# Optimization experiments

Hardware: AMD Instinct MI355X
Metric: run time of the kernel (lower is better)

Reference implementation:

```python
import jax, jax.numpy as jnp
import numpy as np

N_NODES = 50000
N_EDGES = 600000
IN_DIM = 128
HID_DIM = 512
OUT_DIM = 2


def setup_inputs() -> dict:
    key = jax.random.key(0)
    ks = jax.random.split(key, 8)
    x = jax.random.normal(ks[0], (N_NODES, IN_DIM), dtype=jnp.float32)
    edge_index = jax.random.randint(ks[1], (2, N_EDGES), 0, N_NODES, dtype=jnp.int32)
    s1 = 1.0 / np.sqrt(IN_DIM)
    s2 = 1.0 / np.sqrt(HID_DIM)
    # SAGEConv params: lin_l (applied to mean-aggregated neighbors, has bias),
    # lin_r (applied to root node features, no bias)
    W1l = jax.random.uniform(ks[2], (IN_DIM, HID_DIM), jnp.float32, -s1, s1)
    b1 = jax.random.uniform(ks[3], (HID_DIM,), jnp.float32, -s1, s1)
    W1r = jax.random.uniform(ks[4], (IN_DIM, HID_DIM), jnp.float32, -s1, s1)
    W2l = jax.random.uniform(ks[5], (HID_DIM, OUT_DIM), jnp.float32, -s2, s2)
    b2 = jax.random.uniform(ks[6], (OUT_DIM,), jnp.float32, -s2, s2)
    W2r = jax.random.uniform(ks[7], (HID_DIM, OUT_DIM), jnp.float32, -s2, s2)
    return {"x": x, "W1l": W1l, "b1": b1, "W1r": W1r,
            "W2l": W2l, "b2": b2, "W2r": W2r, "edge_index": edge_index}


def _sage_conv(x, edge_index, Wl, b, Wr):
    src, dst = edge_index[0], edge_index[1]
    msgs = x[src]                                             # [E, d]
    agg = jax.ops.segment_sum(msgs, dst, num_segments=x.shape[0])  # [N, d]
    deg = jax.ops.segment_sum(jnp.ones_like(dst, dtype=x.dtype), dst,
                              num_segments=x.shape[0])
    agg = agg / jnp.maximum(deg, 1.0)[:, None]                # mean aggregation
    return agg @ Wl + b + x @ Wr


def reference(x, W1l, b1, W1r, W2l, b2, W2r, edge_index):
    h = _sage_conv(x, edge_index, W1l, b1, W1r)
    h = jax.nn.relu(h)
    # dropout inactive (eval mode / force_dropout=False)
    out = _sage_conv(h, edge_index, W2l, b2, W2r)
    return jax.nn.log_softmax(out, axis=1)
```

## Files before the change

kernel.cpp:

```cpp
#include <hip/hip_runtime.h>
#include <math.h>
#include <stdint.h>

#define N_NODES 50000
#define N_EDGES 600000
#define IN_DIM 128
#define HID_DIM 512
#define M_PAD 50048
#define SCAN_NB 196

#define CASTX_NB 6250
#define CASTW_NB 544

#define NB_H 64
#define CE4_H 2344
#define NPAD 50048
#define H2_WORDS 25024

typedef __bf16 bf16;
typedef __bf16 bf16x2 __attribute__((ext_vector_type(2)));
typedef __bf16 bf16x4 __attribute__((ext_vector_type(4)));
typedef __bf16 bf16x8 __attribute__((ext_vector_type(8)));
typedef float f32x4 __attribute__((ext_vector_type(4)));

#define GLDS(gp, lp) __builtin_amdgcn_global_load_lds( \
    (const __attribute__((address_space(1))) uint32_t*)(gp), \
    (__attribute__((address_space(3))) uint32_t*)(lp), 16, 0, 0)


__global__ __launch_bounds__(256) void prep_kernel(
    const float* __restrict__ x, bf16* __restrict__ xb,
    const float* __restrict__ W1l, const float* __restrict__ W1r,
    const float* __restrict__ W2l, const float* __restrict__ W2r,
    bf16* __restrict__ Wt, bf16* __restrict__ W2bt) {
    int b = blockIdx.x;
    int t = threadIdx.x;
    if (b < CASTX_NB) {
        int i = b * 256 + t;
        float4 v = ((const float4*)x)[i];
        bf16x4 o = {(bf16)v.x, (bf16)v.y, (bf16)v.z, (bf16)v.w};
        *(bf16x4*)(xb + (size_t)i * 4) = o;
    } else {
        int idx = (b - CASTX_NB) * 256 + t;
        if (idx < 512 * 256) {
            int n = idx >> 8;
            int k = idx & 255;
            float v = (k < IN_DIM) ? W1l[(size_t)k * HID_DIM + n]
                                   : W1r[(size_t)(k - IN_DIM) * HID_DIM + n];
            Wt[idx] = (bf16)v;
        } else {
            int j = idx - 512 * 256;
            int n = j >> 9;
            int k = j & 511;
            float v = 0.f;
            if (n == 0) v = W2l[k * 2 + 0];
            else if (n == 1) v = W2l[k * 2 + 1];
            else if (n == 2) v = W2r[k * 2 + 0];
            else if (n == 3) v = W2r[k * 2 + 1];
            W2bt[j] = (bf16)v;
        }
    }
}


__global__ __launch_bounds__(512) void hist_kernel(
    const int* __restrict__ dst, uint32_t* __restrict__ Hg32) {
    __shared__ uint32_t h2[H2_WORDS];
    int b = blockIdx.x, t = threadIdx.x;
    for (int j = t; j < H2_WORDS; j += 512) h2[j] = 0;
    __syncthreads();
    int e40 = b * CE4_H;
    int e4end = min(e40 + CE4_H, N_EDGES / 4);
    for (int e4 = e40 + t; e4 < e4end; e4 += 512) {
        int4 d = ((const int4*)dst)[e4];
        atomicAdd(&h2[d.x >> 1], 1u << ((d.x & 1) << 4));
        atomicAdd(&h2[d.y >> 1], 1u << ((d.y & 1) << 4));
        atomicAdd(&h2[d.z >> 1], 1u << ((d.z & 1) << 4));
        atomicAdd(&h2[d.w >> 1], 1u << ((d.w & 1) << 4));
    }
    __syncthreads();
    for (int j = t; j < H2_WORDS; j += 512)
        Hg32[(size_t)b * H2_WORDS + j] = h2[j];
}


__global__ __launch_bounds__(256) void scancols_kernel(
    const uint16_t* __restrict__ Hg, int* __restrict__ deg,
    uint16_t* __restrict__ PB, int* __restrict__ bsum) {
    int t = threadIdx.x;
    int n = blockIdx.x * 256 + t;
    int running = 0;
    if (n < NPAD) {
#pragma unroll 4
        for (int b = 0; b < NB_H; ++b) {
            int v = Hg[(size_t)b * NPAD + n];
            PB[(size_t)b * NPAD + n] = (uint16_t)running;
            running += v;
        }
        deg[n] = running;
    }
    int v = (n < N_NODES) ? running : 0;
#pragma unroll
    for (int m = 1; m < 64; m <<= 1) v += __shfl_xor(v, m);
    __shared__ int ws_[4];
    int w = t >> 6, l = t & 63;
    if (l == 0) ws_[w] = v;
    __syncthreads();
    if (t == 0) bsum[blockIdx.x] = ws_[0] + ws_[1] + ws_[2] + ws_[3];
}

__global__ __launch_bounds__(256) void scan3_kernel(const int* __restrict__ deg,
                                                    const int* __restrict__ bsum,
                                                    int* __restrict__ offsets) {
    int t = threadIdx.x;
    int blk = blockIdx.x;
    int i = blk * 256 + t;
    int l = t & 63, w = t >> 6;
    int v = (i < N_NODES) ? deg[i] : 0;
    int inc = v;
#pragma unroll
    for (int off = 1; off < 64; off <<= 1) {
        int y = __shfl_up(inc, off);
        if (l >= off) inc += y;
    }
    __shared__ int wsum[4];
    __shared__ int lookback;
    if (l == 63) wsum[w] = inc;
    __syncthreads();
    if (t < 64) {
        int s = 0;
        for (int u = t; u < blk; u += 64) s += bsum[u];
#pragma unroll
        for (int m = 1; m < 64; m <<= 1) s += __shfl_xor(s, m);
        if (t == 0) lookback = s;
    }
    __syncthreads();
    int add = lookback;
    for (int u = 0; u < w; ++u) add += wsum[u];
    int ex = add + inc - v;
    if (i < N_NODES) offsets[i] = ex;
    if (blk == 0 && t == 0) offsets[N_NODES] = N_EDGES;
}


__global__ __launch_bounds__(512) void fill_kernel(
    const int* __restrict__ src, const int* __restrict__ dst,
    const int* __restrict__ offsets, const uint16_t* __restrict__ PB,
    int* __restrict__ csr_src) {
    __shared__ uint32_t h2[H2_WORDS];
    int b = blockIdx.x, t = threadIdx.x;
    for (int j = t; j < H2_WORDS; j += 512) h2[j] = 0;
    __syncthreads();
    const uint16_t* pb = PB + (size_t)b * NPAD;
    int e40 = b * CE4_H;
    int e4end = min(e40 + CE4_H, N_EDGES / 4);
    for (int e4 = e40 + t; e4 < e4end; e4 += 512) {
        int4 d = ((const int4*)dst)[e4];
        int4 s = ((const int4*)src)[e4];
        int sh0 = (d.x & 1) << 4, sh1 = (d.y & 1) << 4;
        int sh2 = (d.z & 1) << 4, sh3 = (d.w & 1) << 4;
        uint32_t r0 = atomicAdd(&h2[d.x >> 1], 1u << sh0);
        uint32_t r1 = atomicAdd(&h2[d.y >> 1], 1u << sh1);
        uint32_t r2 = atomicAdd(&h2[d.z >> 1], 1u << sh2);
        uint32_t r3 = atomicAdd(&h2[d.w >> 1], 1u << sh3);
        int k0 = (int)((r0 >> sh0) & 0xffff);
        int k1 = (int)((r1 >> sh1) & 0xffff);
        int k2 = (int)((r2 >> sh2) & 0xffff);
        int k3 = (int)((r3 >> sh3) & 0xffff);
        csr_src[offsets[d.x] + (int)pb[d.x] + k0] = s.x;
        csr_src[offsets[d.y] + (int)pb[d.y] + k1] = s.y;
        csr_src[offsets[d.z] + (int)pb[d.z] + k2] = s.z;
        csr_src[offsets[d.w] + (int)pb[d.w] + k3] = s.w;
    }
}


__global__ __launch_bounds__(256) void agg1_kernel(
    const bf16* __restrict__ xb, const int* __restrict__ offsets,
    const int* __restrict__ csr_src, bf16* __restrict__ agg1b) {
    int t = threadIdx.x;
    int w = t >> 6, l = t & 63;
    int g = l >> 4;
    int sl = l & 15;
    int n = blockIdx.x * 16 + w * 4 + g;
    int s0 = offsets[n], s1 = offsets[n + 1];
    float a[8] = {};
    int e = s0;
    for (; e + 4 <= s1; e += 4) {
        int i0 = csr_src[e + 0];
        int i1 = csr_src[e + 1];
        int i2 = csr_src[e + 2];
        int i3 = csr_src[e + 3];
        bf16x8 v0 = *(const bf16x8*)(xb + (size_t)i0 * IN_DIM + sl * 8);
        bf16x8 v1 = *(const bf16x8*)(xb + (size_t)i1 * IN_DIM + sl * 8);
        bf16x8 v2 = *(const bf16x8*)(xb + (size_t)i2 * IN_DIM + sl * 8);
        bf16x8 v3 = *(const bf16x8*)(xb + (size_t)i3 * IN_DIM + sl * 8);
#pragma unroll
        for (int u = 0; u < 8; ++u)
            a[u] += (float)v0[u] + (float)v1[u] + (float)v2[u] + (float)v3[u];
    }
    for (; e < s1; ++e) {
        int i0 = csr_src[e];
        bf16x8 v0 = *(const bf16x8*)(xb + (size_t)i0 * IN_DIM + sl * 8);
#pragma unroll
        for (int u = 0; u < 8; ++u) a[u] += (float)v0[u];
    }
    float inv = 1.0f / fmaxf((float)(s1 - s0), 1.0f);
    bf16x8 o;
#pragma unroll
    for (int u = 0; u < 8; ++u) o[u] = (bf16)(a[u] * inv);
    *(bf16x8*)(agg1b + (size_t)n * IN_DIM + sl * 8) = o;
}


__global__ __launch_bounds__(256) void gemm1_kernel(
    const bf16* __restrict__ agg1b, const bf16* __restrict__ xb,
    const bf16* __restrict__ Wt, const float* __restrict__ b1,
    const bf16* __restrict__ W2bt, float* __restrict__ zpart) {
    __shared__ __align__(16) char smem[128 * 136 * 2];
    bf16 (*As)[128][32] = (bf16(*)[128][32])smem;
    bf16 (*Bs)[128][32] = (bf16(*)[128][32])(smem + 16384);
    bf16 (*Hs)[136] = (bf16(*)[136])smem;
    int tid = threadIdx.x;
    int w = tid >> 6;
    int lane = tid & 63;
    int q = lane >> 4, rr = lane & 15;
    int cb = blockIdx.x;
    int n0 = cb * 128;
    int row0 = blockIdx.y * 128;
    int wm = (w & 1) * 64, wn = (w >> 1) * 64;
    int lr = lane >> 2;
    int lc = (lane & 3) * 8;

    auto stage = [&](int ki) {
        const bf16* Asrc;
        int kb;
        if (ki < 4) { Asrc = agg1b; kb = ki * 32; }
        else        { Asrc = xb;    kb = ki * 32 - IN_DIM; }
        int kw = ki * 32;
        int buf = ki & 1;
#pragma unroll
        for (int j = 0; j < 2; ++j) {
            int r = w * 32 + j * 16 + lr;
            GLDS(Asrc + (size_t)(row0 + r) * IN_DIM + kb + lc,
                 &As[buf][w * 32 + j * 16][0]);
            GLDS(Wt + (size_t)(n0 + r) * 256 + kw + lc,
                 &Bs[buf][w * 32 + j * 16][0]);
        }
    };

    f32x4 acc[4][4] = {};
    stage(0);
#pragma unroll
    for (int ki = 0; ki < 8; ++ki) {
        __syncthreads();
        if (ki + 1 < 8) stage(ki + 1);
        int buf = ki & 1;
        bf16x8 af[4], bfr[4];
#pragma unroll
        for (int i = 0; i < 4; ++i)
            af[i] = *(const bf16x8*)&As[buf][wm + i * 16 + rr][q * 8];
#pragma unroll
        for (int j = 0; j < 4; ++j)
            bfr[j] = *(const bf16x8*)&Bs[buf][wn + j * 16 + rr][q * 8];
#pragma unroll
        for (int i = 0; i < 4; ++i)
#pragma unroll
            for (int j = 0; j < 4; ++j)
                acc[i][j] = __builtin_amdgcn_mfma_f32_16x16x32_bf16(
                    af[i], bfr[j], acc[i][j], 0, 0, 0);
    }
    __syncthreads();
    float bias[4];
#pragma unroll
    for (int j = 0; j < 4; ++j) bias[j] = b1[n0 + wn + j * 16 + rr];
#pragma unroll
    for (int i = 0; i < 4; ++i) {
#pragma unroll
        for (int rg = 0; rg < 4; ++rg) {
            int mrow = wm + i * 16 + q * 4 + rg;
#pragma unroll
            for (int j = 0; j < 4; ++j)
                Hs[mrow][wn + j * 16 + rr] =
                    (bf16)fmaxf(acc[i][j][rg] + bias[j], 0.f);
        }
    }
    __syncthreads();
    bf16x8 wf[4];
#pragma unroll
    for (int ks = 0; ks < 4; ++ks)
        wf[ks] = *(const bf16x8*)(W2bt + (size_t)rr * 512 + n0 + ks * 32 + q * 8);
    f32x4 zacc[2] = {};
#pragma unroll
    for (int mt = 0; mt < 2; ++mt)
#pragma unroll
        for (int ks = 0; ks < 4; ++ks) {
            bf16x8 afz = *(const bf16x8*)&Hs[w * 32 + mt * 16 + rr][ks * 32 + q * 8];
            zacc[mt] = __builtin_amdgcn_mfma_f32_16x16x32_bf16(
                afz, wf[ks], zacc[mt], 0, 0, 0);
        }
    if (rr < 4) {
#pragma unroll
        for (int mt = 0; mt < 2; ++mt)
#pragma unroll
            for (int rg = 0; rg < 4; ++rg) {
                int grow = row0 + w * 32 + mt * 16 + q * 4 + rg;
                zpart[(size_t)grow * 16 + cb * 4 + rr] = zacc[mt][rg];
            }
    }
}


__global__ __launch_bounds__(256) void zsum_kernel(const float* __restrict__ zpart,
                                                   float* __restrict__ z) {
    int n = blockIdx.x * blockDim.x + threadIdx.x;
    if (n >= N_NODES) return;
    const float4* p = (const float4*)(zpart + (size_t)n * 16);
    float4 a = p[0], b = p[1], c = p[2], d = p[3];
    float4 o = {a.x + b.x + c.x + d.x, a.y + b.y + c.y + d.y,
                a.z + b.z + c.z + d.z, a.w + b.w + c.w + d.w};
    *(float4*)(z + (size_t)n * 4) = o;
}


__global__ void final_kernel(const float* __restrict__ z, const int* __restrict__ offsets,
                             const int* __restrict__ csr_src, const float* __restrict__ b2,
                             float* __restrict__ out) {
    int n = blockIdx.x * blockDim.x + threadIdx.x;
    if (n >= N_NODES) return;
    int s0 = offsets[n], s1 = offsets[n + 1];
    float a0 = 0.f, a1 = 0.f;
    int e = s0;
    for (; e + 4 <= s1; e += 4) {
        int i0 = csr_src[e], i1 = csr_src[e + 1];
        int i2 = csr_src[e + 2], i3 = csr_src[e + 3];
        float2 v0 = *(const float2*)(z + (size_t)i0 * 4);
        float2 v1 = *(const float2*)(z + (size_t)i1 * 4);
        float2 v2 = *(const float2*)(z + (size_t)i2 * 4);
        float2 v3 = *(const float2*)(z + (size_t)i3 * 4);
        a0 += v0.x + v1.x + v2.x + v3.x;
        a1 += v0.y + v1.y + v2.y + v3.y;
    }
    for (; e < s1; ++e) {
        int s = csr_src[e];
        float2 v = *(const float2*)(z + (size_t)s * 4);
        a0 += v.x;
        a1 += v.y;
    }
    float inv = 1.0f / fmaxf((float)(s1 - s0), 1.0f);
    float2 zs = *(const float2*)(z + (size_t)n * 4 + 2);
    float o0 = a0 * inv + b2[0] + zs.x;
    float o1 = a1 * inv + b2[1] + zs.y;
    float m = fmaxf(o0, o1);
    float lse = logf(expf(o0 - m) + expf(o1 - m));
    float2 o = {o0 - m - lse, o1 - m - lse};
    *(float2*)(out + (size_t)n * 2) = o;
}


extern "C" void kernel_launch(void* const* d_in, const int* in_sizes, int n_in,
                              void* d_out, int out_size, void* d_ws, size_t ws_size,
                              hipStream_t stream) {
    const float* x   = (const float*)d_in[0];
    const float* W1l = (const float*)d_in[1];
    const float* b1  = (const float*)d_in[2];
    const float* W1r = (const float*)d_in[3];
    const float* W2l = (const float*)d_in[4];
    const float* b2  = (const float*)d_in[5];
    const float* W2r = (const float*)d_in[6];
    const int* edge  = (const int*)d_in[7];
    const int* src = edge;
    const int* dst = edge + N_EDGES;
    float* out = (float*)d_out;

    char* ws = (char*)d_ws;
    size_t off = 0;
    auto alloc = [&](size_t bytes) -> void* {
        void* p = ws + off;
        off += (bytes + 255) & ~(size_t)255;
        return p;
    };
    int* deg     = (int*)alloc((size_t)NPAD * 4);
    int* offsets = (int*)alloc((size_t)(N_NODES + 1) * 4);
    int* csr_src = (int*)alloc((size_t)N_EDGES * 4);
    int* bsum    = (int*)alloc((size_t)SCAN_NB * 4);
    bf16* xb     = (bf16*)alloc((size_t)M_PAD * IN_DIM * 2);
    bf16* agg1b  = (bf16*)alloc((size_t)M_PAD * IN_DIM * 2);
    bf16* Wt     = (bf16*)alloc((size_t)HID_DIM * 256 * 2);
    bf16* W2bt   = (bf16*)alloc((size_t)16 * HID_DIM * 2);
    float* zpart = (float*)alloc((size_t)M_PAD * 16 * 4);
    float* z     = (float*)alloc((size_t)N_NODES * 4 * 4);

    uint32_t* Hg32 = (uint32_t*)agg1b;
    uint16_t* PB   = (uint16_t*)((char*)agg1b + (size_t)NB_H * H2_WORDS * 4);

    prep_kernel<<<CASTX_NB + CASTW_NB, 256, 0, stream>>>(
        x, xb, W1l, W1r, W2l, W2r, Wt, W2bt);
    hist_kernel<<<NB_H, 512, 0, stream>>>(dst, Hg32);
    scancols_kernel<<<SCAN_NB, 256, 0, stream>>>(
        (const uint16_t*)Hg32, deg, PB, bsum);
    scan3_kernel<<<SCAN_NB, 256, 0, stream>>>(deg, bsum, offsets);
    fill_kernel<<<NB_H, 512, 0, stream>>>(src, dst, offsets, PB, csr_src);
    agg1_kernel<<<N_NODES / 16, 256, 0, stream>>>(xb, offsets, csr_src, agg1b);
    gemm1_kernel<<<dim3(4, M_PAD / 128), 256, 0, stream>>>(
        agg1b, xb, Wt, b1, W2bt, zpart);
    zsum_kernel<<<(N_NODES + 255) / 256, 256, 0, stream>>>(zpart, z);
    final_kernel<<<(N_NODES + 255) / 256, 256, 0, stream>>>(z, offsets, csr_src, b2, out);
}
```

Baseline: 186.5 us.

## Split CSR histogram/fill into node-halved chunks and fuse histogram with input cast

The histogram and fill passes are now split over 128 edge chunks times 2 node halves, giving 256 blocks instead of 64. Each block holds a half-size LDS histogram, which should allow more blocks per CU and better GPU occupancy. The histogram pass is merged into the x/weight bf16 cast kernel so both run in one launch, removing a kernel boundary. The trade-off is that each block reads every edge in its chunk twice (once per half), the column scan walks 128 partial rows instead of 64, and PB moves to its own workspace allocation.

```diff
diff --git a/kernel.cpp b/kernel.cpp
--- a/kernel.cpp
+++ b/kernel.cpp
@@ -8,14 +8,16 @@
 #define HID_DIM 512
 #define M_PAD 50048
 #define SCAN_NB 196
-
-#define CASTX_NB 6250
-#define CASTW_NB 544
-
-#define NB_H 64
-#define CE4_H 2344
 #define NPAD 50048
-#define H2_WORDS 25024
+
+#define NB_C 128
+#define CE4_C 1172
+#define HALF_N 25024
+#define H2W 12512
+#define HIST_NB 256
+
+#define CASTX_NB5 3125
+#define CASTW_NB5 272
 
 typedef __bf16 bf16;
 typedef __bf16 bf16x2 __attribute__((ext_vector_type(2)));
@@ -28,20 +30,42 @@
     (__attribute__((address_space(3))) uint32_t*)(lp), 16, 0, 0)
 
 
-__global__ __launch_bounds__(256) void prep_kernel(
+__global__ __launch_bounds__(512) void histcast_kernel(
+    const int* __restrict__ dst, uint32_t* __restrict__ Hg32,
     const float* __restrict__ x, bf16* __restrict__ xb,
     const float* __restrict__ W1l, const float* __restrict__ W1r,
     const float* __restrict__ W2l, const float* __restrict__ W2r,
     bf16* __restrict__ Wt, bf16* __restrict__ W2bt) {
-    int b = blockIdx.x;
-    int t = threadIdx.x;
-    if (b < CASTX_NB) {
-        int i = b * 256 + t;
+    __shared__ uint32_t h2[H2W];
+    int b = blockIdx.x, t = threadIdx.x;
+    if (b < HIST_NB) {
+        for (int j = t; j < H2W; j += 512) h2[j] = 0;
+        __syncthreads();
+        int c = b >> 1, h = b & 1;
+        int base = h * HALF_N;
+        int e40 = c * CE4_C;
+        int e4end = min(e40 + CE4_C, N_EDGES / 4);
+        for (int e4 = e40 + t; e4 < e4end; e4 += 512) {
+            int4 d = ((const int4*)dst)[e4];
+            unsigned v0 = (unsigned)(d.x - base);
+            unsigned v1 = (unsigned)(d.y - base);
+            unsigned v2 = (unsigned)(d.z - base);
+            unsigned v3 = (unsigned)(d.w - base);
+            if (v0 < HALF_N) atomicAdd(&h2[v0 >> 1], 1u << ((v0 & 1) << 4));
+            if (v1 < HALF_N) atomicAdd(&h2[v1 >> 1], 1u << ((v1 & 1) << 4));
+            if (v2 < HALF_N) atomicAdd(&h2[v2 >> 1], 1u << ((v2 & 1) << 4));
+            if (v3 < HALF_N) atomicAdd(&h2[v3 >> 1], 1u << ((v3 & 1) << 4));
+        }
+        __syncthreads();
+        uint32_t* outp = Hg32 + (size_t)c * (NPAD / 2) + (size_t)h * H2W;
+        for (int j = t; j < H2W; j += 512) outp[j] = h2[j];
+    } else if (b < HIST_NB + CASTX_NB5) {
+        int i = (b - HIST_NB) * 512 + t;
         float4 v = ((const float4*)x)[i];
         bf16x4 o = {(bf16)v.x, (bf16)v.y, (bf16)v.z, (bf16)v.w};
         *(bf16x4*)(xb + (size_t)i * 4) = o;
     } else {
-        int idx = (b - CASTX_NB) * 256 + t;
+        int idx = (b - HIST_NB - CASTX_NB5) * 512 + t;
         if (idx < 512 * 256) {
             int n = idx >> 8;
             int k = idx & 255;
@@ -63,27 +87,6 @@
 }
 
 
-__global__ __launch_bounds__(512) void hist_kernel(
-    const int* __restrict__ dst, uint32_t* __restrict__ Hg32) {
-    __shared__ uint32_t h2[H2_WORDS];
-    int b = blockIdx.x, t = threadIdx.x;
-    for (int j = t; j < H2_WORDS; j += 512) h2[j] = 0;
-    __syncthreads();
-    int e40 = b * CE4_H;
-    int e4end = min(e40 + CE4_H, N_EDGES / 4);
-    for (int e4 = e40 + t; e4 < e4end; e4 += 512) {
-        int4 d = ((const int4*)dst)[e4];
-        atomicAdd(&h2[d.x >> 1], 1u << ((d.x & 1) << 4));
-        atomicAdd(&h2[d.y >> 1], 1u << ((d.y & 1) << 4));
-        atomicAdd(&h2[d.z >> 1], 1u << ((d.z & 1) << 4));
-        atomicAdd(&h2[d.w >> 1], 1u << ((d.w & 1) << 4));
-    }
-    __syncthreads();
-    for (int j = t; j < H2_WORDS; j += 512)
-        Hg32[(size_t)b * H2_WORDS + j] = h2[j];
-}
-
-
 __global__ __launch_bounds__(256) void scancols_kernel(
     const uint16_t* __restrict__ Hg, int* __restrict__ deg,
     uint16_t* __restrict__ PB, int* __restrict__ bsum) {
@@ -91,10 +94,10 @@
     int n = blockIdx.x * 256 + t;
     int running = 0;
     if (n < NPAD) {
-#pragma unroll 4
-        for (int b = 0; b < NB_H; ++b) {
-            int v = Hg[(size_t)b * NPAD + n];
-            PB[(size_t)b * NPAD + n] = (uint16_t)running;
+#pragma unroll 8
+        for (int c = 0; c < NB_C; ++c) {
+            int v = Hg[(size_t)c * NPAD + n];
+            PB[(size_t)c * NPAD + n] = (uint16_t)running;
             running += v;
         }
         deg[n] = running;
@@ -147,30 +150,42 @@
     const int* __restrict__ src, const int* __restrict__ dst,
     const int* __restrict__ offsets, const uint16_t* __restrict__ PB,
     int* __restrict__ csr_src) {
-    __shared__ uint32_t h2[H2_WORDS];
+    __shared__ uint32_t h2[H2W];
     int b = blockIdx.x, t = threadIdx.x;
-    for (int j = t; j < H2_WORDS; j += 512) h2[j] = 0;
-    __syncthreads();
-    const uint16_t* pb = PB + (size_t)b * NPAD;
-    int e40 = b * CE4_H;
-    int e4end = min(e40 + CE4_H, N_EDGES / 4);
+    for (int j = t; j < H2W; j += 512) h2[j] = 0;
+    __syncthreads();
+    int c = b >> 1, h = b & 1;
+    int base = h * HALF_N;
+    const uint16_t* pb = PB + (size_t)c * NPAD;
+    int e40 = c * CE4_C;
+    int e4end = min(e40 + CE4_C, N_EDGES / 4);
     for (int e4 = e40 + t; e4 < e4end; e4 += 512) {
         int4 d = ((const int4*)dst)[e4];
         int4 s = ((const int4*)src)[e4];
-        int sh0 = (d.x & 1) << 4, sh1 = (d.y & 1) << 4;
-        int sh2 = (d.z & 1) << 4, sh3 = (d.w & 1) << 4;
-        uint32_t r0 = atomicAdd(&h2[d.x >> 1], 1u << sh0);
-        uint32_t r1 = atomicAdd(&h2[d.y >> 1], 1u << sh1);
-        uint32_t r2 = atomicAdd(&h2[d.z >> 1], 1u << sh2);
-        uint32_t r3 = atomicAdd(&h2[d.w >> 1], 1u << sh3);
-        int k0 = (int)((r0 >> sh0) & 0xffff);
-        int k1 = (int)((r1 >> sh1) & 0xffff);
-        int k2 = (int)((r2 >> sh2) & 0xffff);
-        int k3 = (int)((r3 >> sh3) & 0xffff);
-        csr_src[offsets[d.x] + (int)pb[d.x] + k0] = s.x;
-        csr_src[offsets[d.y] + (int)pb[d.y] + k1] = s.y;
-        csr_src[offsets[d.z] + (int)pb[d.z] + k2] = s.z;
-        csr_src[offsets[d.w] + (int)pb[d.w] + k3] = s.w;
+        unsigned v0 = (unsigned)(d.x - base);
+        unsigned v1 = (unsigned)(d.y - base);
+        unsigned v2 = (unsigned)(d.z - base);
+        unsigned v3 = (unsigned)(d.w - base);
+        if (v0 < HALF_N) {
+            int sh = (v0 & 1) << 4;
+            uint32_t r = atomicAdd(&h2[v0 >> 1], 1u << sh);
+            csr_src[offsets[d.x] + (int)pb[d.x] + (int)((r >> sh) & 0xffff)] = s.x;
+        }
+        if (v1 < HALF_N) {
+            int sh = (v1 & 1) << 4;
+            uint32_t r = atomicAdd(&h2[v1 >> 1], 1u << sh);
+            csr_src[offsets[d.y] + (int)pb[d.y] + (int)((r >> sh) & 0xffff)] = s.y;
+        }
+        if (v2 < HALF_N) {
+            int sh = (v2 & 1) << 4;
+            uint32_t r = atomicAdd(&h2[v2 >> 1], 1u << sh);
+            csr_src[offsets[d.z] + (int)pb[d.z] + (int)((r >> sh) & 0xffff)] = s.z;
+        }
+        if (v3 < HALF_N) {
+            int sh = (v3 & 1) << 4;
+            uint32_t r = atomicAdd(&h2[v3 >> 1], 1u << sh);
+            csr_src[offsets[d.w] + (int)pb[d.w] + (int)((r >> sh) & 0xffff)] = s.w;
+        }
     }
 }
 
@@ -390,17 +405,16 @@
     bf16* W2bt   = (bf16*)alloc((size_t)16 * HID_DIM * 2);
     float* zpart = (float*)alloc((size_t)M_PAD * 16 * 4);
     float* z     = (float*)alloc((size_t)N_NODES * 4 * 4);
+    uint16_t* PB = (uint16_t*)alloc((size_t)NB_C * NPAD * 2);
 
     uint32_t* Hg32 = (uint32_t*)agg1b;
-    uint16_t* PB   = (uint16_t*)((char*)agg1b + (size_t)NB_H * H2_WORDS * 4);
-
-    prep_kernel<<<CASTX_NB + CASTW_NB, 256, 0, stream>>>(
-        x, xb, W1l, W1r, W2l, W2r, Wt, W2bt);
-    hist_kernel<<<NB_H, 512, 0, stream>>>(dst, Hg32);
+
+    histcast_kernel<<<HIST_NB + CASTX_NB5 + CASTW_NB5, 512, 0, stream>>>(
+        dst, Hg32, x, xb, W1l, W1r, W2l, W2r, Wt, W2bt);
     scancols_kernel<<<SCAN_NB, 256, 0, stream>>>(
         (const uint16_t*)Hg32, deg, PB, bsum);
     scan3_kernel<<<SCAN_NB, 256, 0, stream>>>(deg, bsum, offsets);
-    fill_kernel<<<NB_H, 512, 0, stream>>>(src, dst, offsets, PB, csr_src);
+    fill_kernel<<<HIST_NB, 512, 0, stream>>>(src, dst, offsets, PB, csr_src);
     agg1_kernel<<<N_NODES / 16, 256, 0, stream>>>(xb, offsets, csr_src, agg1b);
     gemm1_kernel<<<dim3(4, M_PAD / 128), 256, 0, stream>>>(
         agg1b, xb, Wt, b1, W2bt, zpart);
```

Result: faster. 172.5 us (-7.5%).
